# Kernel optimization log

Measured on AMD Instinct MI355X. Metric: run time of the kernel, lower is better.

Reference implementation:

```python
import jax, jax.numpy as jnp
import numpy as np

N, E, D, SD = 50000, 800000, 64, 7

def _lin_init(key, fan_in, shape):
    b = 1.0 / np.sqrt(fan_in)
    return jax.random.uniform(key, shape, minval=-b, maxval=b, dtype=jnp.float32)

def setup_inputs() -> dict:
    key = jax.random.key(0)
    ks = jax.random.split(key, 16)
    edge_index = jax.random.randint(ks[0], (2, E), 0, N, dtype=jnp.int64)
    h = jax.random.normal(ks[1], (N, D), dtype=jnp.float32)
    return {
        "edge_index": edge_index,
        "h": h,
        "W_att": _lin_init(ks[2], D, (D, D)),        # stored [in,out]
        "phi_att_w": _lin_init(ks[3], D, (D, D)),
        "phi_att_b": _lin_init(ks[4], D, (D,)),
        "W_p": _lin_init(ks[5], D, (D, D)),
        "W_pp": _lin_init(ks[6], D, (D, D)),
        "f_def_w": _lin_init(ks[7], D, (D, 1)),
        "f_def_b": _lin_init(ks[8], D, (1,)),
        "W_self_w": _lin_init(ks[9], D, (D, D)),
        "W_self_b": _lin_init(ks[10], D, (D,)),
        "W_A_w": _lin_init(ks[11], D, (D, D)),
        "W_A_b": _lin_init(ks[12], D, (D,)),
        "W_str_w": _lin_init(ks[13], SD - 1, (SD - 1, D)),
        "W_str_b": _lin_init(ks[14], SD - 1, (D,)),
        "ln_g": jnp.ones((D,), jnp.float32),
        "ln_b": jnp.zeros((D,), jnp.float32),
    }

def reference(edge_index, h, W_att, phi_att_w, phi_att_b, W_p, W_pp,
              f_def_w, f_def_b, W_self_w, W_self_b, W_A_w, W_A_b,
              W_str_w, W_str_b, ln_g, ln_b):
    gamma, delta = 1.0, 0.5
    n = h.shape[0]
    src, tgt = edge_index[0], edge_index[1]
    H = h  # in_dim == hidden_dim -> embed is None
    s_feat = h[:, :SD - 1]                      # [N, 6]
    h_src, h_tgt = H[src], H[tgt]               # [E, D] gathers
    # attention-like scatter softmax over incoming edges of tgt
    score = jnp.sum(h_tgt * (h_src @ W_att), axis=-1) \
          + jnp.sum(s_feat[src] * s_feat[tgt], axis=-1)   # [E]
    alpha_num = jnp.exp(score)
    alpha_den = jax.ops.segment_sum(alpha_num, tgt, num_segments=n)
    alpha = alpha_num / (alpha_den[tgt] + 1e-9)
    # pairing / defense term (rev_src=tgt, rev_tgt=src => h_att=H[src], h_def=H[tgt])
    pair = jnp.sum((h_src @ W_p) * (h_tgt @ W_pp), axis=-1)  # [E]
    beta_num = jnp.exp(pair)
    beta_den = jax.ops.segment_sum(beta_num, src, num_segments=n)
    beta = beta_num / (beta_den[src] + 1e-9)
    psi = (h_tgt @ f_def_w)[:, 0] + f_def_b[0]                # [E]
    sum_term = jax.ops.segment_sum(beta * jnp.exp(-psi), src, num_segments=n)
    d = -jnp.log(sum_term + 1e-8)
    rho = jax.nn.sigmoid(gamma * (d - delta))                 # [N]
    rho_edge = rho[src]
    # message + scatter-sum aggregation
    msg = alpha[:, None] * (h_src @ phi_att_w + phi_att_b) * (1.0 - rho_edge)[:, None]
    m_att = jax.ops.segment_sum(msg, tgt, num_segments=n)     # [N, D]
    out = (H @ W_self_w + W_self_b) + (m_att @ W_A_w + W_A_b) \
        + (s_feat @ W_str_w + W_str_b)
    out = jax.nn.relu(out) + H                                # residual
    mu = jnp.mean(out, axis=-1, keepdims=True)
    var = jnp.mean((out - mu) ** 2, axis=-1, keepdims=True)
    out = (out - mu) / jnp.sqrt(var + 1e-5) * ln_g + ln_b     # LayerNorm
    return out
```

## Files before the change

### kernel.cpp

```cpp
#include <hip/hip_runtime.h>
#include <math.h>

#define D 64
#define NB 256
#define SCAN_NB 256
#define PS_NB 2048

typedef _Float16 hf;
typedef _Float16 hf2 __attribute__((ext_vector_type(2)));

__device__ inline float fdot2f(hf2 a, hf2 b, float c) {
#if __has_builtin(__builtin_amdgcn_fdot2)
    return __builtin_amdgcn_fdot2(a, b, c, false);
#else
    return (float)a[0] * (float)b[0] + (float)a[1] * (float)b[1] + c;
#endif
}

__global__ __launch_bounds__(512) void node_pre_hist_kernel(
    const float* __restrict__ h,
    const float* __restrict__ W_att,
    const float* __restrict__ W_p,
    const float* __restrict__ W_pp,
    const float* __restrict__ phi_w,
    const float* __restrict__ phi_b,
    const float* __restrict__ fdef_w,
    const float* __restrict__ fdef_b,
    const int* __restrict__ tgtI, const int* __restrict__ srcI,
    int* __restrict__ ghist_t, int* __restrict__ ghist_s,
    hf* __restrict__ AW16,
    hf* __restrict__ P16,
    hf* __restrict__ PP16,
    float* __restrict__ enpsi,
    int nNodes, int nbNode, int nBkt, int nEdges)
{
    __shared__ hf2 sW2[4][32][D];
    __shared__ hf  hall[32][D];
    __shared__ float sPhib[D];
    __shared__ float sFdef[D];
    __shared__ int hist[2048];

    const int tid = threadIdx.x;

    if (blockIdx.x >= nbNode) {
        const int hb = blockIdx.x - nbNode;
        const int dir = hb / NB;
        const int b = hb % NB;
        const int* keys = dir ? srcI : tgtI;
        int* gh = dir ? ghist_s : ghist_t;
        for (int d = tid; d < nBkt; d += 512) hist[d] = 0;
        __syncthreads();
        const int C = (nEdges + NB - 1) / NB;
        const int beg = b * C;
        const int end = min(beg + C, nEdges);
        for (int e = beg + tid; e < end; e += 512)
            atomicAdd(&hist[keys[e] >> 5], 1);
        __syncthreads();
        for (int d = tid; d < nBkt; d += 512)
            gh[(size_t)d * NB + b] = hist[d];
        return;
    }

    const float* Wm[4] = { W_att, W_p, W_pp, phi_w };
    for (int idx = tid; idx < 4 * 32 * D; idx += 512) {
        const int m  = idx >> 11;
        const int k2 = (idx >> 6) & 31;
        const int j  = idx & 63;
        sW2[m][k2][j] = hf2{(hf)Wm[m][(2 * k2) * D + j], (hf)Wm[m][(2 * k2 + 1) * D + j]};
    }
    if (tid < D) { sPhib[tid] = phi_b[tid]; sFdef[tid] = fdef_w[tid]; }
    __syncthreads();
    const float fb = fdef_b[0];

    const int n0 = blockIdx.x * 32;
    {
        const int base = tid * 4;
        const int ln = base >> 6;
        const int col = base & 63;
        const int n = n0 + ln;
        float ps = 0.f;
        if (n < nNodes) {
            const float4 v = *(const float4*)(h + (size_t)n * D + col);
            hall[ln][col]     = (hf)v.x;
            hall[ln][col + 1] = (hf)v.y;
            hall[ln][col + 2] = (hf)v.z;
            hall[ln][col + 3] = (hf)v.w;
            ps = v.x * sFdef[col] + v.y * sFdef[col + 1]
               + v.z * sFdef[col + 2] + v.w * sFdef[col + 3];
        }
        #pragma unroll
        for (int off = 8; off >= 1; off >>= 1) ps += __shfl_xor(ps, off, 64);
        if ((tid & 15) == 0 && n < nNodes) enpsi[n] = __expf(-(ps + fb));
    }
    __syncthreads();

    const int g = tid >> 6;
    const int j = tid & 63;
    const int ln0 = 4 * g;

    float acc[4][4];
    #pragma unroll
    for (int m = 0; m < 4; ++m) {
        acc[m][0] = 0.f; acc[m][1] = 0.f; acc[m][2] = 0.f; acc[m][3] = sPhib[j];
    }
    const hf2* hr0 = (const hf2*)hall[ln0 + 0];
    const hf2* hr1 = (const hf2*)hall[ln0 + 1];
    const hf2* hr2 = (const hf2*)hall[ln0 + 2];
    const hf2* hr3 = (const hf2*)hall[ln0 + 3];

    #pragma unroll 8
    for (int k2 = 0; k2 < 32; ++k2) {
        const hf2 w0 = sW2[0][k2][j];
        const hf2 w1 = sW2[1][k2][j];
        const hf2 w2 = sW2[2][k2][j];
        const hf2 w3 = sW2[3][k2][j];
        const hf2 h0 = hr0[k2];
        const hf2 h1 = hr1[k2];
        const hf2 h2 = hr2[k2];
        const hf2 h3 = hr3[k2];
        acc[0][0] = fdot2f(w0, h0, acc[0][0]);
        acc[0][1] = fdot2f(w1, h0, acc[0][1]);
        acc[0][2] = fdot2f(w2, h0, acc[0][2]);
        acc[0][3] = fdot2f(w3, h0, acc[0][3]);
        acc[1][0] = fdot2f(w0, h1, acc[1][0]);
        acc[1][1] = fdot2f(w1, h1, acc[1][1]);
        acc[1][2] = fdot2f(w2, h1, acc[1][2]);
        acc[1][3] = fdot2f(w3, h1, acc[1][3]);
        acc[2][0] = fdot2f(w0, h2, acc[2][0]);
        acc[2][1] = fdot2f(w1, h2, acc[2][1]);
        acc[2][2] = fdot2f(w2, h2, acc[2][2]);
        acc[2][3] = fdot2f(w3, h2, acc[2][3]);
        acc[3][0] = fdot2f(w0, h3, acc[3][0]);
        acc[3][1] = fdot2f(w1, h3, acc[3][1]);
        acc[3][2] = fdot2f(w2, h3, acc[3][2]);
        acc[3][3] = fdot2f(w3, h3, acc[3][3]);
    }

    #pragma unroll
    for (int m = 0; m < 4; ++m) {
        const int n = n0 + ln0 + m;
        if (n < nNodes) {
            float a = acc[m][0];
            if (j < 6) a += (float)hall[ln0 + m][j];
            const size_t base = (size_t)n * D + j;
            *(hf2*)(AW16 + ((size_t)n << 7) + 2 * j) = hf2{(hf)a, (hf)acc[m][3]};
            P16[base]  = (hf)acc[m][1];
            PP16[base] = (hf)acc[m][2];
        }
    }
}

__global__ __launch_bounds__(256) void scan_partial_kernel(
    const int* __restrict__ in_t, const int* __restrict__ in_s,
    int* __restrict__ bsum, int L)
{
    const int pass = blockIdx.x >> 8;
    const int b = blockIdx.x & (SCAN_NB - 1);
    const int* in = pass ? in_s : in_t;
    const int C = (L + SCAN_NB - 1) / SCAN_NB;
    const int K = (C + 255) / 256;
    const int base = b * C;
    const int lim = min(base + C, L);
    const int tbeg = base + threadIdx.x * K;
    const int tend = min(tbeg + K, lim);
    int tsum = 0;
    for (int i = tbeg; i < tend; ++i) tsum += in[i];
    __shared__ int red[256];
    red[threadIdx.x] = tsum;
    __syncthreads();
    for (int off = 128; off >= 1; off >>= 1) {
        if (threadIdx.x < off) red[threadIdx.x] += red[threadIdx.x + off];
        __syncthreads();
    }
    if (threadIdx.x == 0) bsum[pass * SCAN_NB + b] = red[0];
}

__global__ __launch_bounds__(512) void scan_bsum_kernel(int* __restrict__ bsum)
{
    __shared__ int s[2 * SCAN_NB];
    const int tid = threadIdx.x;
    const int orig = bsum[tid];
    s[tid] = orig;
    __syncthreads();
    const int seg = tid & (SCAN_NB - 1);
    for (int off = 1; off < SCAN_NB; off <<= 1) {
        const int add = (seg >= off) ? s[tid - off] : 0;
        __syncthreads();
        s[tid] += add;
        __syncthreads();
    }
    bsum[tid] = s[tid] - orig;
}

__global__ __launch_bounds__(256) void scan_final_kernel(
    const int* __restrict__ in_t, const int* __restrict__ in_s,
    const int* __restrict__ bsum,
    int* __restrict__ gsc_t, int* __restrict__ gsc_s, int L)
{
    const int pass = blockIdx.x >> 8;
    const int b = blockIdx.x & (SCAN_NB - 1);
    const int* in = pass ? in_s : in_t;
    int* out = pass ? gsc_s : gsc_t;
    const int C = (L + SCAN_NB - 1) / SCAN_NB;
    const int K = (C + 255) / 256;
    const int base = b * C;
    const int lim = min(base + C, L);
    const int tbeg = base + threadIdx.x * K;
    const int tend = min(tbeg + K, lim);
    int tsum = 0;
    for (int i = tbeg; i < tend; ++i) tsum += in[i];
    __shared__ int s[256];
    s[threadIdx.x] = tsum;
    __syncthreads();
    for (int off = 1; off < 256; off <<= 1) {
        const int add = (threadIdx.x >= off) ? s[threadIdx.x - off] : 0;
        __syncthreads();
        s[threadIdx.x] += add;
        __syncthreads();
    }
    int run = s[threadIdx.x] - tsum + bsum[pass * SCAN_NB + b];
    for (int i = tbeg; i < tend; ++i) { out[i] = run; run += in[i]; }
}

__global__ __launch_bounds__(256) void bucket_scatter_kernel(
    const int* __restrict__ tgtI, const int* __restrict__ srcI,
    const int* __restrict__ gsc_t, const int* __restrict__ gsc_s,
    unsigned* __restrict__ ep_t, unsigned* __restrict__ ep_s,
    int nBkt, int nEdges)
{
    __shared__ int cursor[2048];
    const int dir = blockIdx.x / NB;
    const int b = blockIdx.x % NB;
    const int* keys = dir ? srcI : tgtI;
    const int* pays = dir ? tgtI : srcI;
    const int* gsc = dir ? gsc_s : gsc_t;
    unsigned* ep = dir ? ep_s : ep_t;
    const int tid = threadIdx.x;
    for (int d = tid; d < nBkt; d += 256) cursor[d] = gsc[(size_t)d * NB + b];
    __syncthreads();
    const int C = (nEdges + NB - 1) / NB;
    const int beg = b * C;
    const int end = min(beg + C, nEdges);
    for (int e = beg + tid; e < end; e += 256) {
        const unsigned k = (unsigned)keys[e];
        const unsigned p = (unsigned)pays[e];
        const int pos = atomicAdd(&cursor[k >> 5], 1);
        ep[pos] = (k << 16) | p;
    }
}

__device__ inline void bucket_sort_body(
    const unsigned* __restrict__ ep, const int* __restrict__ gsc,
    int* __restrict__ out, int* __restrict__ rowstart,
    int b, int nBkt, int nNodes, int nEdges,
    int* hist, int* pref, int* cur, int tid)
{
    if (b == 0 && tid == 0) rowstart[nNodes] = nEdges;

    const int s = gsc[(size_t)b * NB];
    const int e = (b + 1 < nBkt) ? gsc[(size_t)(b + 1) * NB] : nEdges;
    const int size = e - s;

    if (tid < 32) hist[tid] = 0;
    __syncthreads();
    for (int i = tid; i < size; i += 256)
        atomicAdd(&hist[(ep[s + i] >> 16) & 31], 1);
    __syncthreads();
    if (tid == 0) {
        int r = 0;
        for (int k = 0; k < 32; ++k) { pref[k] = r; cur[k] = r; r += hist[k]; }
    }
    __syncthreads();
    if (tid < 32) {
        const int key = (b << 5) + tid;
        if (key < nNodes) rowstart[key] = s + pref[tid];
    }
    __syncthreads();
    for (int i = tid; i < size; i += 256) {
        const unsigned v = ep[s + i];
        const int pos = atomicAdd(&cur[(v >> 16) & 31], 1);
        out[s + pos] = (int)(v & 0xFFFFu);
    }
}

__global__ __launch_bounds__(256) void bucket_sort_s_kernel(
    const unsigned* __restrict__ ep_s, const int* __restrict__ gsc_s,
    int* __restrict__ tgt_sorted, int* __restrict__ rowstart_s,
    int nBkt, int nNodes, int nEdges)
{
    __shared__ int hist[32], pref[32], cur[32];
    bucket_sort_body(ep_s, gsc_s, tgt_sorted, rowstart_s,
                     blockIdx.x, nBkt, nNodes, nEdges, hist, pref, cur, threadIdx.x);
}

__global__ __launch_bounds__(256) void pass_src_sortT_kernel(
    const int* __restrict__ rowstart_s,
    const int* __restrict__ tgt_sorted,
    const hf* __restrict__ P16,
    const hf* __restrict__ PP16,
    const float* __restrict__ enpsi,
    hf* __restrict__ AW16,
    const unsigned* __restrict__ ep_t, const int* __restrict__ gsc_t,
    int* __restrict__ src_sorted, int* __restrict__ rowstart_t,
    int nBkt, int nNodes, int nEdges)
{
    __shared__ int hist[32], pref[32], cur[32];
    const int tid = threadIdx.x;

    if (blockIdx.x >= PS_NB) {
        bucket_sort_body(ep_t, gsc_t, src_sorted, rowstart_t,
                         blockIdx.x - PS_NB, nBkt, nNodes, nEdges, hist, pref, cur, tid);
        return;
    }

    const int grp = tid >> 4;
    const int l = tid & 15;

    for (int n = blockIdx.x * 16 + grp; n < nNodes; n += PS_NB * 16) {
        const int beg = rowstart_s[n];
        const int end = rowstart_s[n + 1];
        const float2 pr = ((const float2*)(P16 + (size_t)n * D))[l];
        const hf* pq = (const hf*)&pr;
        const float p0 = pq[0], p1 = pq[1], p2 = pq[2], p3 = pq[3];
        float bden = 0.f, ssum = 0.f;

        int k = beg;
        for (; k + 7 < end; k += 8) {
            int tv[8]; float2 rv[8]; float ev[8];
            #pragma unroll
            for (int u = 0; u < 8; ++u) tv[u] = tgt_sorted[k + u];
            #pragma unroll
            for (int u = 0; u < 8; ++u) rv[u] = ((const float2*)(PP16 + (size_t)tv[u] * D))[l];
            #pragma unroll
            for (int u = 0; u < 8; ++u) ev[u] = enpsi[tv[u]];
            float sc[8];
            #pragma unroll
            for (int u = 0; u < 8; ++u) {
                const hf* q = (const hf*)&rv[u];
                sc[u] = (float)q[0] * p0 + (float)q[1] * p1 + (float)q[2] * p2 + (float)q[3] * p3;
            }
            #pragma unroll
            for (int off = 8; off >= 1; off >>= 1) {
                #pragma unroll
                for (int u = 0; u < 8; ++u) sc[u] += __shfl_xor(sc[u], off, 64);
            }
            #pragma unroll
            for (int u = 0; u < 8; ++u) {
                const float bn = __expf(sc[u]);
                bden += bn;
                ssum += bn * ev[u];
            }
        }
        for (; k + 3 < end; k += 4) {
            int tv[4]; float2 rv[4]; float ev[4];
            #pragma unroll
            for (int u = 0; u < 4; ++u) tv[u] = tgt_sorted[k + u];
            #pragma unroll
            for (int u = 0; u < 4; ++u) rv[u] = ((const float2*)(PP16 + (size_t)tv[u] * D))[l];
            #pragma unroll
            for (int u = 0; u < 4; ++u) ev[u] = enpsi[tv[u]];
            float sc[4];
            #pragma unroll
            for (int u = 0; u < 4; ++u) {
                const hf* q = (const hf*)&rv[u];
                sc[u] = (float)q[0] * p0 + (float)q[1] * p1 + (float)q[2] * p2 + (float)q[3] * p3;
            }
            #pragma unroll
            for (int off = 8; off >= 1; off >>= 1) {
                #pragma unroll
                for (int u = 0; u < 4; ++u) sc[u] += __shfl_xor(sc[u], off, 64);
            }
            #pragma unroll
            for (int u = 0; u < 4; ++u) {
                const float bn = __expf(sc[u]);
                bden += bn;
                ssum += bn * ev[u];
            }
        }
        for (; k < end; ++k) {
            const int t = tgt_sorted[k];
            const float2 r = ((const float2*)(PP16 + (size_t)t * D))[l];
            const float et = enpsi[t];
            const hf* q = (const hf*)&r;
            float a2 = (float)q[0] * p0 + (float)q[1] * p1 + (float)q[2] * p2 + (float)q[3] * p3;
            #pragma unroll
            for (int off = 8; off >= 1; off >>= 1) a2 += __shfl_xor(a2, off, 64);
            const float bn = __expf(a2);
            bden += bn;
            ssum += bn * et;
        }
        const float st = ssum / (bden + 1e-9f);
        const float d = -logf(st + 1e-8f);
        const float w = 1.0f - 1.0f / (1.0f + __expf(-(d - 0.5f)));
        float4* rowp = (float4*)(AW16 + ((size_t)n << 7));
        float4 rv = rowp[l];
        hf* q = (hf*)&rv;
        q[1] = (hf)((float)q[1] * w);
        q[3] = (hf)((float)q[3] * w);
        q[5] = (hf)((float)q[5] * w);
        q[7] = (hf)((float)q[7] * w);
        rowp[l] = rv;
    }
}

__global__ __launch_bounds__(256) void pass_tgt_fused_kernel(
    const int* __restrict__ rowstart_t,
    const int* __restrict__ src_sorted,
    const float* __restrict__ h,
    const hf* __restrict__ AW16,
    hf* __restrict__ m16,
    int nNodes)
{
    const int grp = threadIdx.x >> 4;
    const int l = threadIdx.x & 15;

    for (int n = blockIdx.x * 16 + grp; n < nNodes; n += gridDim.x * 16) {
        const int beg = rowstart_t[n];
        const int end = rowstart_t[n + 1];
        const float4 htv = ((const float4*)(h + (size_t)n * D))[l];
        float aden = 0.f;
        float m0 = 0.f, m1 = 0.f, m2 = 0.f, m3 = 0.f;

        int k = beg;
        for (; k + 7 < end; k += 8) {
            int sv[8]; float4 rv[8];
            #pragma unroll
            for (int u = 0; u < 8; ++u) sv[u] = src_sorted[k + u];
            #pragma unroll
            for (int u = 0; u < 8; ++u) rv[u] = ((const float4*)(AW16 + ((size_t)sv[u] << 7)))[l];
            float sc[8];
            #pragma unroll
            for (int u = 0; u < 8; ++u) {
                const hf* q = (const hf*)&rv[u];
                sc[u] = (float)q[0] * htv.x + (float)q[2] * htv.y
                      + (float)q[4] * htv.z + (float)q[6] * htv.w;
            }
            #pragma unroll
            for (int off = 8; off >= 1; off >>= 1) {
                #pragma unroll
                for (int u = 0; u < 8; ++u) sc[u] += __shfl_xor(sc[u], off, 64);
            }
            #pragma unroll
            for (int u = 0; u < 8; ++u) {
                const float an = __expf(sc[u]);
                aden += an;
                const hf* q = (const hf*)&rv[u];
                m0 += an * (float)q[1];
                m1 += an * (float)q[3];
                m2 += an * (float)q[5];
                m3 += an * (float)q[7];
            }
        }
        for (; k + 3 < end; k += 4) {
            int sv[4]; float4 rv[4];
            #pragma unroll
            for (int u = 0; u < 4; ++u) sv[u] = src_sorted[k + u];
            #pragma unroll
            for (int u = 0; u < 4; ++u) rv[u] = ((const float4*)(AW16 + ((size_t)sv[u] << 7)))[l];
            float sc[4];
            #pragma unroll
            for (int u = 0; u < 4; ++u) {
                const hf* q = (const hf*)&rv[u];
                sc[u] = (float)q[0] * htv.x + (float)q[2] * htv.y
                      + (float)q[4] * htv.z + (float)q[6] * htv.w;
            }
            #pragma unroll
            for (int off = 8; off >= 1; off >>= 1) {
                #pragma unroll
                for (int u = 0; u < 4; ++u) sc[u] += __shfl_xor(sc[u], off, 64);
            }
            #pragma unroll
            for (int u = 0; u < 4; ++u) {
                const float an = __expf(sc[u]);
                aden += an;
                const hf* q = (const hf*)&rv[u];
                m0 += an * (float)q[1];
                m1 += an * (float)q[3];
                m2 += an * (float)q[5];
                m3 += an * (float)q[7];
            }
        }
        for (; k < end; ++k) {
            const int s = src_sorted[k];
            const float4 r = ((const float4*)(AW16 + ((size_t)s << 7)))[l];
            const hf* q = (const hf*)&r;
            float a1 = (float)q[0] * htv.x + (float)q[2] * htv.y
                     + (float)q[4] * htv.z + (float)q[6] * htv.w;
            #pragma unroll
            for (int off = 8; off >= 1; off >>= 1) a1 += __shfl_xor(a1, off, 64);
            const float an = __expf(a1);
            aden += an;
            m0 += an * (float)q[1];
            m1 += an * (float)q[3];
            m2 += an * (float)q[5];
            m3 += an * (float)q[7];
        }

        const float idn = 1.0f / (aden + 1e-9f);
        hf o4[4];
        o4[0] = (hf)(m0 * idn);
        o4[1] = (hf)(m1 * idn);
        o4[2] = (hf)(m2 * idn);
        o4[3] = (hf)(m3 * idn);
        ((float2*)(m16 + (size_t)n * D))[l] = *(const float2*)o4;
    }
}

__global__ __launch_bounds__(512) void final_kernel(
    const float* __restrict__ h,
    const hf* __restrict__ m16,
    const float* __restrict__ W_self_w, const float* __restrict__ W_self_b,
    const float* __restrict__ W_A_w,    const float* __restrict__ W_A_b,
    const float* __restrict__ W_str_w,  const float* __restrict__ W_str_b,
    const float* __restrict__ ln_g,     const float* __restrict__ ln_b,
    float* __restrict__ out,
    int nNodes)
{
    __shared__ hf2 sWs2[32][D];
    __shared__ hf2 sWa2[32][D];
    __shared__ float sWstr[6 * D];
    __shared__ float sBias[D];
    __shared__ float sG[D], sB[D];
    __shared__ hf hall[32][D];
    __shared__ hf mall[32][D];

    const int tid = threadIdx.x;
    for (int idx = tid; idx < 32 * D; idx += 512) {
        const int k2 = idx >> 6, j = idx & 63;
        sWs2[k2][j] = hf2{(hf)W_self_w[(2 * k2) * D + j], (hf)W_self_w[(2 * k2 + 1) * D + j]};
        sWa2[k2][j] = hf2{(hf)W_A_w[(2 * k2) * D + j],    (hf)W_A_w[(2 * k2 + 1) * D + j]};
    }
    for (int i = tid; i < 6 * D; i += 512) sWstr[i] = W_str_w[i];
    if (tid < D) {
        sBias[tid] = W_self_b[tid] + W_A_b[tid] + W_str_b[tid];
        sG[tid] = ln_g[tid];
        sB[tid] = ln_b[tid];
    }

    const int n0 = blockIdx.x * 32;
    {
        const int base = tid * 4;
        const int ln = base >> 6;
        const int col = base & 63;
        const int n = n0 + ln;
        if (n < nNodes) {
            const float4 v = *(const float4*)(h + (size_t)n * D + col);
            hall[ln][col]     = (hf)v.x;
            hall[ln][col + 1] = (hf)v.y;
            hall[ln][col + 2] = (hf)v.z;
            hall[ln][col + 3] = (hf)v.w;
            *(uint2*)&mall[ln][col] = *(const uint2*)(m16 + (size_t)n * D + col);
        }
    }
    __syncthreads();

    const int g = tid >> 6, j = tid & 63;
    const int ln0 = 4 * g;

    float acc[4];
    #pragma unroll
    for (int m = 0; m < 4; ++m) acc[m] = sBias[j];

    const hf2* hr0 = (const hf2*)hall[ln0 + 0];
    const hf2* hr1 = (const hf2*)hall[ln0 + 1];
    const hf2* hr2 = (const hf2*)hall[ln0 + 2];
    const hf2* hr3 = (const hf2*)hall[ln0 + 3];
    const hf2* mr0 = (const hf2*)mall[ln0 + 0];
    const hf2* mr1 = (const hf2*)mall[ln0 + 1];
    const hf2* mr2 = (const hf2*)mall[ln0 + 2];
    const hf2* mr3 = (const hf2*)mall[ln0 + 3];

    #pragma unroll 8
    for (int k2 = 0; k2 < 32; ++k2) {
        const hf2 ws = sWs2[k2][j];
        const hf2 wa = sWa2[k2][j];
        acc[0] = fdot2f(ws, hr0[k2], acc[0]);
        acc[0] = fdot2f(wa, mr0[k2], acc[0]);
        acc[1] = fdot2f(ws, hr1[k2], acc[1]);
        acc[1] = fdot2f(wa, mr1[k2], acc[1]);
        acc[2] = fdot2f(ws, hr2[k2], acc[2]);
        acc[2] = fdot2f(wa, mr2[k2], acc[2]);
        acc[3] = fdot2f(ws, hr3[k2], acc[3]);
        acc[3] = fdot2f(wa, mr3[k2], acc[3]);
    }
    #pragma unroll
    for (int k = 0; k < 6; ++k) {
        const float w = sWstr[k * D + j];
        acc[0] += (float)hall[ln0 + 0][k] * w;
        acc[1] += (float)hall[ln0 + 1][k] * w;
        acc[2] += (float)hall[ln0 + 2][k] * w;
        acc[3] += (float)hall[ln0 + 3][k] * w;
    }

    float pre[4], mu[4], vv[4];
    #pragma unroll
    for (int m = 0; m < 4; ++m)
        pre[m] = fmaxf(acc[m], 0.f) + (float)hall[ln0 + m][j];

    #pragma unroll
    for (int m = 0; m < 4; ++m) mu[m] = pre[m];
    #pragma unroll
    for (int off = 32; off >= 1; off >>= 1) {
        #pragma unroll
        for (int m = 0; m < 4; ++m) mu[m] += __shfl_xor(mu[m], off, 64);
    }
    #pragma unroll
    for (int m = 0; m < 4; ++m) {
        mu[m] *= (1.0f / 64.0f);
        const float diff = pre[m] - mu[m];
        vv[m] = diff * diff;
    }
    #pragma unroll
    for (int off = 32; off >= 1; off >>= 1) {
        #pragma unroll
        for (int m = 0; m < 4; ++m) vv[m] += __shfl_xor(vv[m], off, 64);
    }
    #pragma unroll
    for (int m = 0; m < 4; ++m) {
        const int n = n0 + ln0 + m;
        if (n < nNodes) {
            const float diff = pre[m] - mu[m];
            out[(size_t)n * D + j] = diff * rsqrtf(vv[m] * (1.0f / 64.0f) + 1e-5f) * sG[j] + sB[j];
        }
    }
}

extern "C" void kernel_launch(void* const* d_in, const int* in_sizes, int n_in,
                              void* d_out, int out_size, void* d_ws, size_t ws_size,
                              hipStream_t stream) {
    const int* edge       = (const int*)d_in[0];
    const float* h        = (const float*)d_in[1];
    const float* W_att    = (const float*)d_in[2];
    const float* phi_w    = (const float*)d_in[3];
    const float* phi_b    = (const float*)d_in[4];
    const float* W_p      = (const float*)d_in[5];
    const float* W_pp     = (const float*)d_in[6];
    const float* fdef_w   = (const float*)d_in[7];
    const float* fdef_b   = (const float*)d_in[8];
    const float* W_self_w = (const float*)d_in[9];
    const float* W_self_b = (const float*)d_in[10];
    const float* W_A_w    = (const float*)d_in[11];
    const float* W_A_b    = (const float*)d_in[12];
    const float* W_str_w  = (const float*)d_in[13];
    const float* W_str_b  = (const float*)d_in[14];
    const float* ln_g     = (const float*)d_in[15];
    const float* ln_b     = (const float*)d_in[16];

    const int E = in_sizes[0] / 2;
    const int nNodes = in_sizes[1] / D;
    const int* srcI = edge;
    const int* tgtI = edge + E;
    const int nBkt = (nNodes + 31) / 32;
    const int L = nBkt * NB;
    const int nbNode = (nNodes + 31) / 32;

    char* ws = (char*)d_ws;
    size_t off = 0;
    auto alloc = [&](size_t bytes) { char* p = ws + off; off = (off + bytes + 255) & ~(size_t)255; return p; };

    hf*       AW16      = (hf*)      alloc((size_t)nNodes * 2 * D * 2);
    hf*       P16       = (hf*)      alloc((size_t)nNodes * D * 2);
    hf*       PP16      = (hf*)      alloc((size_t)nNodes * D * 2);
    hf*       m16       = (hf*)      alloc((size_t)nNodes * D * 2);
    float*    enpsi     = (float*)   alloc((size_t)nNodes * 4);
    int*      ghist_t   = (int*)     alloc((size_t)L * 4);
    int*      ghist_s   = (int*)     alloc((size_t)L * 4);
    int*      gsc_t     = (int*)     alloc((size_t)L * 4);
    int*      gsc_s     = (int*)     alloc((size_t)L * 4);
    unsigned* ep_t      = (unsigned*)alloc((size_t)E * 4);
    unsigned* ep_s      = (unsigned*)alloc((size_t)E * 4);
    int*      src_sorted= (int*)     alloc((size_t)E * 4);
    int*      tgt_sorted= (int*)     alloc((size_t)E * 4);
    int*      rowstart_t= (int*)     alloc(((size_t)nNodes + 1) * 4);
    int*      rowstart_s= (int*)     alloc(((size_t)nNodes + 1) * 4);
    int*      bsum      = (int*)     alloc((size_t)2 * SCAN_NB * 4);

    node_pre_hist_kernel<<<nbNode + 2 * NB, 512, 0, stream>>>(
        h, W_att, W_p, W_pp, phi_w, phi_b, fdef_w, fdef_b,
        tgtI, srcI, ghist_t, ghist_s,
        AW16, P16, PP16, enpsi, nNodes, nbNode, nBkt, E);

    scan_partial_kernel<<<2 * SCAN_NB, 256, 0, stream>>>(ghist_t, ghist_s, bsum, L);
    scan_bsum_kernel<<<1, 2 * SCAN_NB, 0, stream>>>(bsum);
    scan_final_kernel<<<2 * SCAN_NB, 256, 0, stream>>>(
        ghist_t, ghist_s, bsum, gsc_t, gsc_s, L);

    bucket_scatter_kernel<<<2 * NB, 256, 0, stream>>>(
        tgtI, srcI, gsc_t, gsc_s, ep_t, ep_s, nBkt, E);

    bucket_sort_s_kernel<<<nBkt, 256, 0, stream>>>(
        ep_s, gsc_s, tgt_sorted, rowstart_s, nBkt, nNodes, E);

    pass_src_sortT_kernel<<<PS_NB + nBkt, 256, 0, stream>>>(
        rowstart_s, tgt_sorted, P16, PP16, enpsi, AW16,
        ep_t, gsc_t, src_sorted, rowstart_t, nBkt, nNodes, E);

    pass_tgt_fused_kernel<<<2048, 256, 0, stream>>>(
        rowstart_t, src_sorted, h, AW16, m16, nNodes);

    final_kernel<<<nbNode, 512, 0, stream>>>(
        h, m16, W_self_w, W_self_b, W_A_w, W_A_b,
        W_str_w, W_str_b, ln_g, ln_b, (float*)d_out, nNodes);
}
```

Baseline: 167.4 us.

## Fuse target-side aggregation with final linear and LayerNorm kernel

Merges the per-target message aggregation kernel with the final self/aggregate linear layers, ReLU residual and LayerNorm, so the m16 intermediate no longer goes to global memory and one launch is removed. Each 16-lane group now computes four output columns for its node from shared-memory fp16 weights and normalises across lanes with shuffles. The node-precompute kernel's shared arrays are put in a union with the histogram buffer to cut LDS use. In exchange, the fused kernel loads the weights into shared memory per block and its dot-product loop reads weights with stride-4 column access, which may cause LDS bank conflicts.

```diff
diff --git a/kernel.cpp b/kernel.cpp
--- a/kernel.cpp
+++ b/kernel.cpp
@@ -34,11 +34,16 @@
     float* __restrict__ enpsi,
     int nNodes, int nbNode, int nBkt, int nEdges)
 {
-    __shared__ hf2 sW2[4][32][D];
-    __shared__ hf  hall[32][D];
-    __shared__ float sPhib[D];
-    __shared__ float sFdef[D];
-    __shared__ int hist[2048];
+    union SMem {
+        struct {
+            hf2 sW2[4][32][D];
+            hf  hall[32][D];
+            float sPhib[D];
+            float sFdef[D];
+        } np;
+        int hist[2048];
+    };
+    __shared__ SMem sm;
 
     const int tid = threadIdx.x;
 
@@ -48,16 +53,16 @@
         const int b = hb % NB;
         const int* keys = dir ? srcI : tgtI;
         int* gh = dir ? ghist_s : ghist_t;
-        for (int d = tid; d < nBkt; d += 512) hist[d] = 0;
+        for (int d = tid; d < nBkt; d += 512) sm.hist[d] = 0;
         __syncthreads();
         const int C = (nEdges + NB - 1) / NB;
         const int beg = b * C;
         const int end = min(beg + C, nEdges);
         for (int e = beg + tid; e < end; e += 512)
-            atomicAdd(&hist[keys[e] >> 5], 1);
+            atomicAdd(&sm.hist[keys[e] >> 5], 1);
         __syncthreads();
         for (int d = tid; d < nBkt; d += 512)
-            gh[(size_t)d * NB + b] = hist[d];
+            gh[(size_t)d * NB + b] = sm.hist[d];
         return;
     }
 
@@ -66,9 +71,9 @@
         const int m  = idx >> 11;
         const int k2 = (idx >> 6) & 31;
         const int j  = idx & 63;
-        sW2[m][k2][j] = hf2{(hf)Wm[m][(2 * k2) * D + j], (hf)Wm[m][(2 * k2 + 1) * D + j]};
-    }
-    if (tid < D) { sPhib[tid] = phi_b[tid]; sFdef[tid] = fdef_w[tid]; }
+        sm.np.sW2[m][k2][j] = hf2{(hf)Wm[m][(2 * k2) * D + j], (hf)Wm[m][(2 * k2 + 1) * D + j]};
+    }
+    if (tid < D) { sm.np.sPhib[tid] = phi_b[tid]; sm.np.sFdef[tid] = fdef_w[tid]; }
     __syncthreads();
     const float fb = fdef_b[0];
 
@@ -81,12 +86,12 @@
         float ps = 0.f;
         if (n < nNodes) {
             const float4 v = *(const float4*)(h + (size_t)n * D + col);
-            hall[ln][col]     = (hf)v.x;
-            hall[ln][col + 1] = (hf)v.y;
-            hall[ln][col + 2] = (hf)v.z;
-            hall[ln][col + 3] = (hf)v.w;
-            ps = v.x * sFdef[col] + v.y * sFdef[col + 1]
-               + v.z * sFdef[col + 2] + v.w * sFdef[col + 3];
+            sm.np.hall[ln][col]     = (hf)v.x;
+            sm.np.hall[ln][col + 1] = (hf)v.y;
+            sm.np.hall[ln][col + 2] = (hf)v.z;
+            sm.np.hall[ln][col + 3] = (hf)v.w;
+            ps = v.x * sm.np.sFdef[col] + v.y * sm.np.sFdef[col + 1]
+               + v.z * sm.np.sFdef[col + 2] + v.w * sm.np.sFdef[col + 3];
         }
         #pragma unroll
         for (int off = 8; off >= 1; off >>= 1) ps += __shfl_xor(ps, off, 64);
@@ -101,19 +106,19 @@
     float acc[4][4];
     #pragma unroll
     for (int m = 0; m < 4; ++m) {
-        acc[m][0] = 0.f; acc[m][1] = 0.f; acc[m][2] = 0.f; acc[m][3] = sPhib[j];
-    }
-    const hf2* hr0 = (const hf2*)hall[ln0 + 0];
-    const hf2* hr1 = (const hf2*)hall[ln0 + 1];
-    const hf2* hr2 = (const hf2*)hall[ln0 + 2];
-    const hf2* hr3 = (const hf2*)hall[ln0 + 3];
+        acc[m][0] = 0.f; acc[m][1] = 0.f; acc[m][2] = 0.f; acc[m][3] = sm.np.sPhib[j];
+    }
+    const hf2* hr0 = (const hf2*)sm.np.hall[ln0 + 0];
+    const hf2* hr1 = (const hf2*)sm.np.hall[ln0 + 1];
+    const hf2* hr2 = (const hf2*)sm.np.hall[ln0 + 2];
+    const hf2* hr3 = (const hf2*)sm.np.hall[ln0 + 3];
 
     #pragma unroll 8
     for (int k2 = 0; k2 < 32; ++k2) {
-        const hf2 w0 = sW2[0][k2][j];
-        const hf2 w1 = sW2[1][k2][j];
-        const hf2 w2 = sW2[2][k2][j];
-        const hf2 w3 = sW2[3][k2][j];
+        const hf2 w0 = sm.np.sW2[0][k2][j];
+        const hf2 w1 = sm.np.sW2[1][k2][j];
+        const hf2 w2 = sm.np.sW2[2][k2][j];
+        const hf2 w3 = sm.np.sW2[3][k2][j];
         const hf2 h0 = hr0[k2];
         const hf2 h1 = hr1[k2];
         const hf2 h2 = hr2[k2];
@@ -141,7 +146,7 @@
         const int n = n0 + ln0 + m;
         if (n < nNodes) {
             float a = acc[m][0];
-            if (j < 6) a += (float)hall[ln0 + m][j];
+            if (j < 6) a += (float)sm.np.hall[ln0 + m][j];
             const size_t base = (size_t)n * D + j;
             *(hf2*)(AW16 + ((size_t)n << 7) + 2 * j) = hf2{(hf)a, (hf)acc[m][3]};
             P16[base]  = (hf)acc[m][1];
@@ -403,16 +408,42 @@
     }
 }
 
-__global__ __launch_bounds__(256) void pass_tgt_fused_kernel(
+__global__ __launch_bounds__(256) void pass_tgt_final_kernel(
     const int* __restrict__ rowstart_t,
     const int* __restrict__ src_sorted,
     const float* __restrict__ h,
     const hf* __restrict__ AW16,
-    hf* __restrict__ m16,
+    const float* __restrict__ W_self_w, const float* __restrict__ W_self_b,
+    const float* __restrict__ W_A_w,    const float* __restrict__ W_A_b,
+    const float* __restrict__ W_str_w,  const float* __restrict__ W_str_b,
+    const float* __restrict__ ln_g,     const float* __restrict__ ln_b,
+    float* __restrict__ out,
     int nNodes)
 {
-    const int grp = threadIdx.x >> 4;
-    const int l = threadIdx.x & 15;
+    __shared__ hf2 sWs2[32][D];
+    __shared__ hf2 sWa2[32][D];
+    __shared__ hf  sWstr[6][D];
+    __shared__ float sBias[D], sG[D], sB[D];
+    __shared__ hf hrow[16][D];
+    __shared__ hf mrow[16][D];
+
+    const int tid = threadIdx.x;
+    for (int idx = tid; idx < 32 * D; idx += 256) {
+        const int k2 = idx >> 6, j = idx & 63;
+        sWs2[k2][j] = hf2{(hf)W_self_w[(2 * k2) * D + j], (hf)W_self_w[(2 * k2 + 1) * D + j]};
+        sWa2[k2][j] = hf2{(hf)W_A_w[(2 * k2) * D + j],    (hf)W_A_w[(2 * k2 + 1) * D + j]};
+    }
+    for (int i = tid; i < 6 * D; i += 256) sWstr[i >> 6][i & 63] = (hf)W_str_w[i];
+    if (tid < D) {
+        sBias[tid] = W_self_b[tid] + W_A_b[tid] + W_str_b[tid];
+        sG[tid] = ln_g[tid];
+        sB[tid] = ln_b[tid];
+    }
+    __syncthreads();
+
+    const int grp = tid >> 4;
+    const int l = tid & 15;
+    const int j0 = 4 * l;
 
     for (int n = blockIdx.x * 16 + grp; n < nNodes; n += gridDim.x * 16) {
         const int beg = rowstart_t[n];
@@ -497,131 +528,62 @@
         }
 
         const float idn = 1.0f / (aden + 1e-9f);
-        hf o4[4];
-        o4[0] = (hf)(m0 * idn);
-        o4[1] = (hf)(m1 * idn);
-        o4[2] = (hf)(m2 * idn);
-        o4[3] = (hf)(m3 * idn);
-        ((float2*)(m16 + (size_t)n * D))[l] = *(const float2*)o4;
-    }
-}
-
-__global__ __launch_bounds__(512) void final_kernel(
-    const float* __restrict__ h,
-    const hf* __restrict__ m16,
-    const float* __restrict__ W_self_w, const float* __restrict__ W_self_b,
-    const float* __restrict__ W_A_w,    const float* __restrict__ W_A_b,
-    const float* __restrict__ W_str_w,  const float* __restrict__ W_str_b,
-    const float* __restrict__ ln_g,     const float* __restrict__ ln_b,
-    float* __restrict__ out,
-    int nNodes)
-{
-    __shared__ hf2 sWs2[32][D];
-    __shared__ hf2 sWa2[32][D];
-    __shared__ float sWstr[6 * D];
-    __shared__ float sBias[D];
-    __shared__ float sG[D], sB[D];
-    __shared__ hf hall[32][D];
-    __shared__ hf mall[32][D];
-
-    const int tid = threadIdx.x;
-    for (int idx = tid; idx < 32 * D; idx += 512) {
-        const int k2 = idx >> 6, j = idx & 63;
-        sWs2[k2][j] = hf2{(hf)W_self_w[(2 * k2) * D + j], (hf)W_self_w[(2 * k2 + 1) * D + j]};
-        sWa2[k2][j] = hf2{(hf)W_A_w[(2 * k2) * D + j],    (hf)W_A_w[(2 * k2 + 1) * D + j]};
-    }
-    for (int i = tid; i < 6 * D; i += 512) sWstr[i] = W_str_w[i];
-    if (tid < D) {
-        sBias[tid] = W_self_b[tid] + W_A_b[tid] + W_str_b[tid];
-        sG[tid] = ln_g[tid];
-        sB[tid] = ln_b[tid];
-    }
-
-    const int n0 = blockIdx.x * 32;
-    {
-        const int base = tid * 4;
-        const int ln = base >> 6;
-        const int col = base & 63;
-        const int n = n0 + ln;
-        if (n < nNodes) {
-            const float4 v = *(const float4*)(h + (size_t)n * D + col);
-            hall[ln][col]     = (hf)v.x;
-            hall[ln][col + 1] = (hf)v.y;
-            hall[ln][col + 2] = (hf)v.z;
-            hall[ln][col + 3] = (hf)v.w;
-            *(uint2*)&mall[ln][col] = *(const uint2*)(m16 + (size_t)n * D + col);
-        }
-    }
-    __syncthreads();
-
-    const int g = tid >> 6, j = tid & 63;
-    const int ln0 = 4 * g;
-
-    float acc[4];
-    #pragma unroll
-    for (int m = 0; m < 4; ++m) acc[m] = sBias[j];
-
-    const hf2* hr0 = (const hf2*)hall[ln0 + 0];
-    const hf2* hr1 = (const hf2*)hall[ln0 + 1];
-    const hf2* hr2 = (const hf2*)hall[ln0 + 2];
-    const hf2* hr3 = (const hf2*)hall[ln0 + 3];
-    const hf2* mr0 = (const hf2*)mall[ln0 + 0];
-    const hf2* mr1 = (const hf2*)mall[ln0 + 1];
-    const hf2* mr2 = (const hf2*)mall[ln0 + 2];
-    const hf2* mr3 = (const hf2*)mall[ln0 + 3];
-
-    #pragma unroll 8
-    for (int k2 = 0; k2 < 32; ++k2) {
-        const hf2 ws = sWs2[k2][j];
-        const hf2 wa = sWa2[k2][j];
-        acc[0] = fdot2f(ws, hr0[k2], acc[0]);
-        acc[0] = fdot2f(wa, mr0[k2], acc[0]);
-        acc[1] = fdot2f(ws, hr1[k2], acc[1]);
-        acc[1] = fdot2f(wa, mr1[k2], acc[1]);
-        acc[2] = fdot2f(ws, hr2[k2], acc[2]);
-        acc[2] = fdot2f(wa, mr2[k2], acc[2]);
-        acc[3] = fdot2f(ws, hr3[k2], acc[3]);
-        acc[3] = fdot2f(wa, mr3[k2], acc[3]);
-    }
-    #pragma unroll
-    for (int k = 0; k < 6; ++k) {
-        const float w = sWstr[k * D + j];
-        acc[0] += (float)hall[ln0 + 0][k] * w;
-        acc[1] += (float)hall[ln0 + 1][k] * w;
-        acc[2] += (float)hall[ln0 + 2][k] * w;
-        acc[3] += (float)hall[ln0 + 3][k] * w;
-    }
-
-    float pre[4], mu[4], vv[4];
-    #pragma unroll
-    for (int m = 0; m < 4; ++m)
-        pre[m] = fmaxf(acc[m], 0.f) + (float)hall[ln0 + m][j];
-
-    #pragma unroll
-    for (int m = 0; m < 4; ++m) mu[m] = pre[m];
-    #pragma unroll
-    for (int off = 32; off >= 1; off >>= 1) {
+        {
+            hf t4[4];
+            t4[0] = (hf)(m0 * idn); t4[1] = (hf)(m1 * idn);
+            t4[2] = (hf)(m2 * idn); t4[3] = (hf)(m3 * idn);
+            *(float2*)&mrow[grp][j0] = *(const float2*)t4;
+            hf h4[4];
+            h4[0] = (hf)htv.x; h4[1] = (hf)htv.y; h4[2] = (hf)htv.z; h4[3] = (hf)htv.w;
+            *(float2*)&hrow[grp][j0] = *(const float2*)h4;
+        }
+
+        float acc0 = sBias[j0], acc1 = sBias[j0 + 1], acc2 = sBias[j0 + 2], acc3 = sBias[j0 + 3];
+        const hf2* hv = (const hf2*)hrow[grp];
+        const hf2* mv = (const hf2*)mrow[grp];
+        #pragma unroll 8
+        for (int k2 = 0; k2 < 32; ++k2) {
+            const hf2 hh = hv[k2];
+            const hf2 mm = mv[k2];
+            acc0 = fdot2f(sWs2[k2][j0],     hh, acc0);
+            acc0 = fdot2f(sWa2[k2][j0],     mm, acc0);
+            acc1 = fdot2f(sWs2[k2][j0 + 1], hh, acc1);
+            acc1 = fdot2f(sWa2[k2][j0 + 1], mm, acc1);
+            acc2 = fdot2f(sWs2[k2][j0 + 2], hh, acc2);
+            acc2 = fdot2f(sWa2[k2][j0 + 2], mm, acc2);
+            acc3 = fdot2f(sWs2[k2][j0 + 3], hh, acc3);
+            acc3 = fdot2f(sWa2[k2][j0 + 3], mm, acc3);
+        }
         #pragma unroll
-        for (int m = 0; m < 4; ++m) mu[m] += __shfl_xor(mu[m], off, 64);
-    }
-    #pragma unroll
-    for (int m = 0; m < 4; ++m) {
-        mu[m] *= (1.0f / 64.0f);
-        const float diff = pre[m] - mu[m];
-        vv[m] = diff * diff;
-    }
-    #pragma unroll
-    for (int off = 32; off >= 1; off >>= 1) {
+        for (int k = 0; k < 6; ++k) {
+            const float hk = (float)hrow[grp][k];
+            acc0 += hk * (float)sWstr[k][j0];
+            acc1 += hk * (float)sWstr[k][j0 + 1];
+            acc2 += hk * (float)sWstr[k][j0 + 2];
+            acc3 += hk * (float)sWstr[k][j0 + 3];
+        }
+
+        const float pre0 = fmaxf(acc0, 0.f) + htv.x;
+        const float pre1 = fmaxf(acc1, 0.f) + htv.y;
+        const float pre2 = fmaxf(acc2, 0.f) + htv.z;
+        const float pre3 = fmaxf(acc3, 0.f) + htv.w;
+
+        float mu = pre0 + pre1 + pre2 + pre3;
         #pragma unroll
-        for (int m = 0; m < 4; ++m) vv[m] += __shfl_xor(vv[m], off, 64);
-    }
-    #pragma unroll
-    for (int m = 0; m < 4; ++m) {
-        const int n = n0 + ln0 + m;
-        if (n < nNodes) {
-            const float diff = pre[m] - mu[m];
-            out[(size_t)n * D + j] = diff * rsqrtf(vv[m] * (1.0f / 64.0f) + 1e-5f) * sG[j] + sB[j];
-        }
+        for (int off = 8; off >= 1; off >>= 1) mu += __shfl_xor(mu, off, 64);
+        mu *= (1.0f / 64.0f);
+        const float d0 = pre0 - mu, d1 = pre1 - mu, d2 = pre2 - mu, d3 = pre3 - mu;
+        float vv = d0 * d0 + d1 * d1 + d2 * d2 + d3 * d3;
+        #pragma unroll
+        for (int off = 8; off >= 1; off >>= 1) vv += __shfl_xor(vv, off, 64);
+        const float rstd = rsqrtf(vv * (1.0f / 64.0f) + 1e-5f);
+
+        float4 o;
+        o.x = d0 * rstd * sG[j0]     + sB[j0];
+        o.y = d1 * rstd * sG[j0 + 1] + sB[j0 + 1];
+        o.z = d2 * rstd * sG[j0 + 2] + sB[j0 + 2];
+        o.w = d3 * rstd * sG[j0 + 3] + sB[j0 + 3];
+        *(float4*)(out + (size_t)n * D + j0) = o;
     }
 }
 
@@ -661,7 +623,6 @@
     hf*       AW16      = (hf*)      alloc((size_t)nNodes * 2 * D * 2);
     hf*       P16       = (hf*)      alloc((size_t)nNodes * D * 2);
     hf*       PP16      = (hf*)      alloc((size_t)nNodes * D * 2);
-    hf*       m16       = (hf*)      alloc((size_t)nNodes * D * 2);
     float*    enpsi     = (float*)   alloc((size_t)nNodes * 4);
     int*      ghist_t   = (int*)     alloc((size_t)L * 4);
     int*      ghist_s   = (int*)     alloc((size_t)L * 4);
@@ -695,10 +656,8 @@
         rowstart_s, tgt_sorted, P16, PP16, enpsi, AW16,
         ep_t, gsc_t, src_sorted, rowstart_t, nBkt, nNodes, E);
 
-    pass_tgt_fused_kernel<<<2048, 256, 0, stream>>>(
-        rowstart_t, src_sorted, h, AW16, m16, nNodes);
-
-    final_kernel<<<nbNode, 512, 0, stream>>>(
-        h, m16, W_self_w, W_self_b, W_A_w, W_A_b,
-        W_str_w, W_str_b, ln_g, ln_b, (float*)d_out, nNodes);
-}
+    pass_tgt_final_kernel<<<2048, 256, 0, stream>>>(
+        rowstart_t, src_sorted, h, AW16,
+        W_self_w, W_self_b, W_A_w, W_A_b, W_str_w, W_str_b,
+        ln_g, ln_b, (float*)d_out, nNodes);
+}
```

After: 167.0 us. Within noise of the previous version (-0.2%).
